# Optimization experiments

Measured on AMD Instinct MI355X. Metric: run time of the kernel, lower is better.

Reference implementation:

```python
import jax, jax.numpy as jnp
import numpy as np

D_MODEL = 768
NUM_HEADS = 12
D_K = D_MODEL // NUM_HEADS


def setup_inputs() -> dict:
    key = jax.random.key(0)
    k1, k2, k3 = jax.random.split(key, 3)
    s = 1.0 / np.sqrt(D_MODEL)
    return {
        "x": jax.random.normal(k1, (4, 2048, D_MODEL), dtype=jnp.float32),
        "W_qkv": jax.random.normal(k2, (D_MODEL, 3 * D_MODEL), dtype=jnp.float32) * s,
        "b_qkv": jnp.zeros((3 * D_MODEL,), dtype=jnp.float32),
        "W_out": jax.random.normal(k3, (D_MODEL, D_MODEL), dtype=jnp.float32) * s,
        "b_out": jnp.zeros((D_MODEL,), dtype=jnp.float32),
    }


def reference(x, W_qkv, b_qkv, W_out, b_out):
    B, S, _ = x.shape
    # fused QKV projection: [B,S,3*d_model]
    qkv = x @ W_qkv + b_qkv
    # reshape to [B,S,H,3*d_k] then to [B,H,S,3*d_k] (matches torch permute)
    qkv = qkv.reshape(B, S, NUM_HEADS, 3 * D_K).transpose(0, 2, 1, 3)
    q, k, v = jnp.split(qkv, 3, axis=-1)  # each [B,H,S,d_k]
    scale = 1.0 / jnp.sqrt(jnp.float32(D_K))
    scores = jnp.einsum("bhqd,bhkd->bhqk", q, k) * scale
    attn = jax.nn.softmax(scores, axis=-1)
    context = jnp.einsum("bhqk,bhkd->bhqd", attn, v)
    context = context.transpose(0, 2, 1, 3).reshape(B, S, D_MODEL)
    return context @ W_out + b_out
```

## Files before the change

kernel.cpp:

```cpp
#include <hip/hip_runtime.h>
#include <hip/hip_bf16.h>
#include <math.h>

#define D_MODEL 768
#define NUM_HEADS 12
#define D_K 64
#define SEQ 2048
#define BATCH 4
#define QKV_N 2304

#define QSCALE 0.18033688011112042f

typedef _Float16 f16;
typedef f16 f16x4 __attribute__((ext_vector_type(4)));
typedef f16 f16x8 __attribute__((ext_vector_type(8)));
typedef float f32x4 __attribute__((ext_vector_type(4)));

#if __has_builtin(__builtin_amdgcn_exp2f)
#define EXP2F(x) __builtin_amdgcn_exp2f(x)
#else
#define EXP2F(x) __expf(0.6931471805599453f * (x))
#endif

__device__ __forceinline__ void gload_lds16(const f16* g, f16* l) {
  __builtin_amdgcn_global_load_lds(
      (const __attribute__((address_space(1))) void*)g,
      (__attribute__((address_space(3))) void*)l, 16, 0, 0);
}

__device__ inline void xcd_swizzle(int& bx, int& by) {
  const int nx = gridDim.x;
  const int nwg = nx * gridDim.y;
  const int bidlin = blockIdx.y * nx + blockIdx.x;
  const int cpx = nwg >> 3;
  const int wg = (bidlin & 7) * cpx + (bidlin >> 3);
  bx = wg % nx;
  by = wg / nx;
}

__global__ __launch_bounds__(256) void prep_all(
    const float* __restrict__ x, const float* __restrict__ Wq,
    const float* __restrict__ Wo, f16* __restrict__ xh,
    f16* __restrict__ Wqt, f16* __restrict__ Wot) {
  const int bid = blockIdx.x;
  const int tid = threadIdx.x;
  __shared__ f16 t[64][72];

  if (bid < 1536) {
    const int idx = bid * 256 + tid;
#pragma unroll
    for (int i = 0; i < 2; ++i) {
      const size_t c = (size_t)idx + (size_t)i * 393216;
      const float4 a = *(const float4*)(x + c * 8);
      const float4 b = *(const float4*)(x + c * 8 + 4);
      f16x8 h = { (f16)a.x, (f16)a.y, (f16)a.z, (f16)a.w,
                  (f16)b.x, (f16)b.y, (f16)b.z, (f16)b.w };
      *(f16x8*)(xh + c * 8) = h;
    }
    return;
  }

  const float* W;
  f16* Wt;
  int K, N, n0, k0;
  if (bid < 1968) {
    const int tt = bid - 1536;
    W = Wq; Wt = Wqt; K = 768; N = QKV_N;
    n0 = (tt % 36) * 64; k0 = (tt / 36) * 64;
  } else {
    const int tt = bid - 1968;
    W = Wo; Wt = Wot; K = 768; N = D_MODEL;
    n0 = (tt % 12) * 64; k0 = (tt / 12) * 64;
  }

#pragma unroll
  for (int i = 0; i < 4; ++i) {
    const int slot = tid + i * 256;
    const int r = slot >> 4;
    const int c4 = (slot & 15) * 4;
    const float4 v = *(const float4*)(W + (size_t)(k0 + r) * N + n0 + c4);
    t[c4 + 0][r] = (f16)v.x;
    t[c4 + 1][r] = (f16)v.y;
    t[c4 + 2][r] = (f16)v.z;
    t[c4 + 3][r] = (f16)v.w;
  }
  __syncthreads();
#pragma unroll
  for (int i = 0; i < 2; ++i) {
    const int slot = tid + i * 256;
    const int n = slot >> 3;
    const int kc = (slot & 7) * 8;
    *(f16x8*)(Wt + (size_t)(n0 + n) * K + k0 + kc) = *(const f16x8*)(&t[n][kc]);
  }
}

#define GEMM_CORE(A_, B_, K_)                                               \
  __shared__ f16 Als[128 * 32];                                             \
  __shared__ f16 Bls[128 * 32];                                             \
  f32x4 acc[4][4];                                                          \
  _Pragma("unroll") for (int i = 0; i < 4; ++i)                             \
      _Pragma("unroll") for (int j = 0; j < 4; ++j)                         \
          acc[i][j] = (f32x4){0.f, 0.f, 0.f, 0.f};                          \
  const int sr = w * 32 + (lane >> 2);                                      \
  const int sc = (lane & 3) * 8;                                            \
  const f16* gA0 = A_ + (size_t)(bm + sr) * K_ + sc;                        \
  const f16* gA1 = gA0 + (size_t)16 * K_;                                   \
  const f16* gB0 = B_ + (size_t)(bn + sr) * K_ + sc;                        \
  const f16* gB1 = gB0 + (size_t)16 * K_;                                   \
  f16* lA0 = Als + (w * 32) * 32;                                           \
  f16* lA1 = lA0 + 16 * 32;                                                 \
  f16* lB0 = Bls + (w * 32) * 32;                                           \
  f16* lB1 = lB0 + 16 * 32;                                                 \
  for (int k0 = 0; k0 < K_; k0 += 32) {                                     \
    gload_lds16(gA0 + k0, lA0);                                             \
    gload_lds16(gA1 + k0, lA1);                                             \
    gload_lds16(gB0 + k0, lB0);                                             \
    gload_lds16(gB1 + k0, lB1);                                             \
    __syncthreads();                                                        \
    f16x8 af[4], bf[4];                                                     \
    _Pragma("unroll") for (int mi = 0; mi < 4; ++mi)                        \
        af[mi] = *(const f16x8*)(Als + (wr * 64 + mi * 16 + c) * 32 + g * 8); \
    _Pragma("unroll") for (int nj = 0; nj < 4; ++nj)                        \
        bf[nj] = *(const f16x8*)(Bls + (wc * 64 + nj * 16 + c) * 32 + g * 8); \
    _Pragma("unroll") for (int mi = 0; mi < 4; ++mi)                        \
        _Pragma("unroll") for (int nj = 0; nj < 4; ++nj)                    \
            acc[mi][nj] = __builtin_amdgcn_mfma_f32_16x16x32_f16(           \
                af[mi], bf[nj], acc[mi][nj], 0, 0, 0);                      \
    __syncthreads();                                                        \
  }

__global__ __launch_bounds__(256) void gemm_qkv(
    const f16* __restrict__ A, const f16* __restrict__ B,
    const float* __restrict__ bias,
    f16* __restrict__ Qh, f16* __restrict__ Kh, f16* __restrict__ Vt) {
  int bx, by;
  xcd_swizzle(bx, by);
  const int bm = by * 128;
  const int bn = bx * 128;
  const int tid = threadIdx.x;
  const int lane = tid & 63;
  const int w = tid >> 6;
  const int wr = w >> 1;
  const int wc = w & 1;
  const int c = lane & 15;
  const int g = lane >> 4;

  GEMM_CORE(A, B, 768)

  const int crow = g * 4;
  const int ccol = c;
#pragma unroll
  for (int nj = 0; nj < 4; ++nj) {
    const int col = bn + wc * 64 + nj * 16 + ccol;
    const int h = col / 192;
    const int rem = col - h * 192;
    const int sub = rem >> 6;
    const int d = rem & 63;
    const float bv = bias[col];
#pragma unroll
    for (int mi = 0; mi < 4; ++mi) {
      const int tok0 = bm + wr * 64 + mi * 16 + crow;
      const int b = tok0 >> 11;
      const int t0 = tok0 & 2047;
      const int bh = b * NUM_HEADS + h;
      if (sub == 2) {
        f16x4 pv = { (f16)(acc[mi][nj][0] + bv), (f16)(acc[mi][nj][1] + bv),
                     (f16)(acc[mi][nj][2] + bv), (f16)(acc[mi][nj][3] + bv) };
        *(f16x4*)(Vt + ((size_t)bh * 64 + d) * SEQ + t0) = pv;
      } else if (sub == 0) {
#pragma unroll
        for (int r = 0; r < 4; ++r)
          Qh[((size_t)bh * SEQ + t0 + r) * 64 + d] =
              (f16)((acc[mi][nj][r] + bv) * QSCALE);
      } else {
#pragma unroll
        for (int r = 0; r < 4; ++r)
          Kh[((size_t)bh * SEQ + t0 + r) * 64 + d] =
              (f16)(acc[mi][nj][r] + bv);
      }
    }
  }
}

__global__ __launch_bounds__(256) void gemm_out(
    const f16* __restrict__ A, const f16* __restrict__ B,
    const float* __restrict__ bias, float* __restrict__ C) {
  int bx, by;
  xcd_swizzle(bx, by);
  const int bm = by * 128;
  const int bn = bx * 128;
  const int tid = threadIdx.x;
  const int lane = tid & 63;
  const int w = tid >> 6;
  const int wr = w >> 1;
  const int wc = w & 1;
  const int c = lane & 15;
  const int g = lane >> 4;

  GEMM_CORE(A, B, 768)

  const int crow = g * 4;
  const int ccol = c;
#pragma unroll
  for (int nj = 0; nj < 4; ++nj) {
    const int col = bn + wc * 64 + nj * 16 + ccol;
    const float bv = bias[col];
#pragma unroll
    for (int mi = 0; mi < 4; ++mi) {
      const int rbase = bm + wr * 64 + mi * 16 + crow;
#pragma unroll
      for (int r = 0; r < 4; ++r) {
        C[(size_t)(rbase + r) * D_MODEL + col] = acc[mi][nj][r] + bv;
      }
    }
  }
}

#define COMPUTE_TILE(KL_, VL_)                                              \
  {                                                                         \
    f32x4 s_[4];                                                            \
    _Pragma("unroll") for (int mt = 0; mt < 4; ++mt)                        \
        s_[mt] = (f32x4){0.f, 0.f, 0.f, 0.f};                               \
    __builtin_amdgcn_s_setprio(1);                                          \
    _Pragma("unroll") for (int s2 = 0; s2 < 2; ++s2) {                      \
      _Pragma("unroll") for (int mt = 0; mt < 4; ++mt) {                    \
        const int row = mt * 16 + c;                                        \
        const f16x8 kf = *(const f16x8*)(KL_ + row * 64 +                   \
                         ((s2 * 32 + g * 8) ^ ((row & 7) << 3)));           \
        s_[mt] = __builtin_amdgcn_mfma_f32_16x16x32_f16(                    \
            kf, qf[s2], s_[mt], 0, 0, 0);                                   \
      }                                                                     \
    }                                                                       \
    __builtin_amdgcn_s_setprio(0);                                          \
    float tm = -INFINITY;                                                   \
    _Pragma("unroll") for (int mt = 0; mt < 4; ++mt)                        \
        _Pragma("unroll") for (int r = 0; r < 4; ++r)                       \
            tm = fmaxf(tm, s_[mt][r]);                                      \
    tm = fmaxf(tm, __shfl_xor(tm, 16));                                     \
    tm = fmaxf(tm, __shfl_xor(tm, 32));                                     \
    if (!__all(tm <= m_)) {                                                 \
      const float mn2 = fmaxf(m_, tm);                                      \
      const float sc2 = EXP2F(m_ - mn2);                                    \
      m_ = mn2;                                                             \
      l_ *= sc2;                                                            \
      _Pragma("unroll") for (int dt = 0; dt < 4; ++dt) o[dt] *= sc2;        \
    }                                                                       \
    const float mn = m_;                                                    \
    float rs = 0.f;                                                         \
    _Pragma("unroll") for (int mt = 0; mt < 4; ++mt) {                      \
      f32x4 e;                                                              \
      _Pragma("unroll") for (int r = 0; r < 4; ++r) {                       \
        e[r] = EXP2F(s_[mt][r] - mn);                                       \
        rs += e[r];                                                         \
      }                                                                     \
      s_[mt] = e;                                                           \
    }                                                                       \
    rs += __shfl_xor(rs, 16);                                               \
    rs += __shfl_xor(rs, 32);                                               \
    l_ += rs;                                                               \
    _Pragma("unroll") for (int mt = 0; mt < 4; ++mt) {                      \
      f16x4 pk = { (f16)s_[mt][0], (f16)s_[mt][1],                          \
                   (f16)s_[mt][2], (f16)s_[mt][3] };                        \
      *(f16x4*)(&Pl[w][c * 64 + ((mt * 16 + g * 4) ^ ((c & 7) << 3))]) = pk;\
    }                                                                       \
    __builtin_amdgcn_s_setprio(1);                                          \
    _Pragma("unroll") for (int s2 = 0; s2 < 2; ++s2) {                      \
      const f16x8 pf = *(const f16x8*)(&Pl[w][c * 64 +                      \
                        ((s2 * 32 + g * 8) ^ ((c & 7) << 3))]);             \
      _Pragma("unroll") for (int dt = 0; dt < 4; ++dt) {                    \
        const int row = dt * 16 + c;                                        \
        const f16x8 vf = *(const f16x8*)(VL_ + row * 64 +                   \
                         ((s2 * 32 + g * 8) ^ ((row & 7) << 3)));           \
        o[dt] = __builtin_amdgcn_mfma_f32_16x16x32_f16(                     \
            vf, pf, o[dt], 0, 0, 0);                                        \
      }                                                                     \
    }                                                                       \
    __builtin_amdgcn_s_setprio(0);                                          \
  }

__global__ __launch_bounds__(512, 6) void flash_attn_mfma(
    const f16* __restrict__ Qh, const f16* __restrict__ Kh,
    const f16* __restrict__ Vt, f16* __restrict__ ctxh) {
  const int qt = blockIdx.x, h = blockIdx.y, b = blockIdx.z;
  const int bh = b * NUM_HEADS + h;
  const int q0 = qt * 128;
  const int tid = threadIdx.x;
  const int lane = tid & 63;
  const int w = tid >> 6;
  const int c = lane & 15;
  const int g = lane >> 4;

  __shared__ f16 QPl[128 * 64];
  __shared__ f16 Kl[64 * 64];
  __shared__ f16 Vl[64 * 64];
  __shared__ f16 Pl[8][16 * 64];
  f16* Ql = QPl;
  f16* KB = QPl;
  f16* VB = QPl + 64 * 64;

  const f16* Kbase = Kh + (size_t)bh * SEQ * 64;
  const f16* Vbase = Vt + (size_t)bh * 64 * SEQ;

  const int srow = tid >> 3;
  const int sg8 = (tid & 7) * 8;
  const int sswz = sg8 ^ ((srow & 7) << 3);

#pragma unroll
  for (int ii = 0; ii < 2; ++ii) {
    const int slot = tid + ii * 512;
    const int row = slot >> 3;
    const int g8 = (slot & 7) * 8;
    f16x8 hq = *(const f16x8*)(Qh + ((size_t)bh * SEQ + q0 + row) * 64 + g8);
    *(f16x8*)(Ql + row * 64 + (g8 ^ ((row & 7) << 3))) = hq;
  }
  {
    f16x8 hk = *(const f16x8*)(Kbase + (size_t)srow * 64 + sg8);
    *(f16x8*)(Kl + srow * 64 + sswz) = hk;
    f16x8 hv = *(const f16x8*)(Vbase + (size_t)srow * SEQ + sg8);
    *(f16x8*)(Vl + srow * 64 + sswz) = hv;
  }
  __syncthreads();

  f16x8 qf[2];
#pragma unroll
  for (int s = 0; s < 2; ++s) {
    const int row = w * 16 + c;
    qf[s] = *(const f16x8*)(Ql + row * 64 +
                            ((s * 32 + g * 8) ^ ((row & 7) << 3)));
  }
  __syncthreads();

  {
    f16x8 hk = *(const f16x8*)(Kbase + (size_t)64 * 64 + (size_t)srow * 64 + sg8);
    *(f16x8*)(KB + srow * 64 + sswz) = hk;
    f16x8 hv = *(const f16x8*)(Vbase + (size_t)srow * SEQ + 64 + sg8);
    *(f16x8*)(VB + srow * 64 + sswz) = hv;
  }
  __syncthreads();

  f32x4 o[4];
  float m_ = -INFINITY, l_ = 0.f;
#pragma unroll
  for (int dt = 0; dt < 4; ++dt) o[dt] = (f32x4){0.f, 0.f, 0.f, 0.f};

  for (int pt = 0; pt < SEQ / 128; ++pt) {
    f16x8 nkA, nvA, nkB, nvB;
    const bool more = (pt + 1) < SEQ / 128;
    if (more) {
      const int tA = 2 * pt + 2, tB = 2 * pt + 3;
      nkA = *(const f16x8*)(Kbase + (size_t)tA * 64 * 64 + (size_t)srow * 64 + sg8);
      nvA = *(const f16x8*)(Vbase + (size_t)srow * SEQ + tA * 64 + sg8);
      nkB = *(const f16x8*)(Kbase + (size_t)tB * 64 * 64 + (size_t)srow * 64 + sg8);
      nvB = *(const f16x8*)(Vbase + (size_t)srow * SEQ + tB * 64 + sg8);
    }

    COMPUTE_TILE(Kl, Vl)
    COMPUTE_TILE(KB, VB)

    __syncthreads();

    if (more) {
      *(f16x8*)(Kl + srow * 64 + sswz) = nkA;
      *(f16x8*)(Vl + srow * 64 + sswz) = nvA;
      *(f16x8*)(KB + srow * 64 + sswz) = nkB;
      *(f16x8*)(VB + srow * 64 + sswz) = nvB;
    }
    __syncthreads();
  }

  {
    const float inv = 1.f / l_;
    const int q = q0 + w * 16 + c;
#pragma unroll
    for (int dt = 0; dt < 4; ++dt) {
      f16x4 r4 = { (f16)(o[dt][0] * inv), (f16)(o[dt][1] * inv),
                   (f16)(o[dt][2] * inv), (f16)(o[dt][3] * inv) };
      *(f16x4*)(ctxh + ((size_t)(b * SEQ) + q) * D_MODEL + h * 64 +
                dt * 16 + g * 4) = r4;
    }
  }
}

extern "C" void kernel_launch(void* const* d_in, const int* in_sizes, int n_in,
                              void* d_out, int out_size, void* d_ws, size_t ws_size,
                              hipStream_t stream) {
  const float* x     = (const float*)d_in[0];
  const float* W_qkv = (const float*)d_in[1];
  const float* b_qkv = (const float*)d_in[2];
  const float* W_out = (const float*)d_in[3];
  const float* b_out = (const float*)d_in[4];
  float* out = (float*)d_out;

  const int M = BATCH * SEQ;
  const int BH = BATCH * NUM_HEADS;

  f16* xh   = (f16*)d_ws;
  f16* Wqt  = xh + (size_t)M * D_MODEL;
  f16* Wot  = Wqt + (size_t)QKV_N * D_MODEL;
  f16* Qh   = Wot + (size_t)D_MODEL * D_MODEL;
  f16* Kh   = Qh + (size_t)BH * SEQ * 64;
  f16* Vt   = Kh + (size_t)BH * SEQ * 64;
  f16* ctxh = Vt + (size_t)BH * SEQ * 64;

  dim3 block(256);

  hipLaunchKernelGGL(prep_all, dim3(2112), block, 0, stream,
                     x, W_qkv, W_out, xh, Wqt, Wot);

  hipLaunchKernelGGL(gemm_qkv, dim3(QKV_N / 128, M / 128), block, 0, stream,
                     xh, Wqt, b_qkv, Qh, Kh, Vt);

  hipLaunchKernelGGL(flash_attn_mfma, dim3(SEQ / 128, NUM_HEADS, BATCH),
                     dim3(512), 0, stream, Qh, Kh, Vt, ctxh);

  hipLaunchKernelGGL(gemm_out, dim3(D_MODEL / 128, M / 128), block, 0, stream,
                     ctxh, Wot, b_out, out);
}
```

Baseline: 178.1 us.

## Pipeline K/V loads per tile and remap attention grid for L2 locality

The attention loop now handles one 64-key tile per step instead of two. Each step prefetches only the next tile into registers and writes it into the buffer it has just finished with, with one barrier per step. This holds fewer prefetch registers at a time and drops the extra barrier per 128 keys, at the cost of more frequent synchronisation. The 3D grid also becomes a 1D grid whose index interleaves batch-head across the low bits, so blocks that share the same K/V likely land together (presumably the same XCD), aiming for better L2 reuse.

```diff
diff --git a/kernel.cpp b/kernel.cpp
--- a/kernel.cpp
+++ b/kernel.cpp
@@ -216,8 +216,16 @@
   }
 }
 
-#define COMPUTE_TILE(KL_, VL_)                                              \
+#define ATTN_STEP(KL_, VL_, TLOAD_)                                         \
   {                                                                         \
+    f16x8 nk, nv;                                                           \
+    const bool more = (TLOAD_) < SEQ / 64;                                  \
+    if (more) {                                                             \
+      nk = *(const f16x8*)(Kbase + (size_t)(TLOAD_) * 64 * 64 +             \
+                           (size_t)srow * 64 + sg8);                        \
+      nv = *(const f16x8*)(Vbase + (size_t)srow * SEQ + (TLOAD_) * 64 +     \
+                           sg8);                                            \
+    }                                                                       \
     f32x4 s_[4];                                                            \
     _Pragma("unroll") for (int mt = 0; mt < 4; ++mt)                        \
         s_[mt] = (f32x4){0.f, 0.f, 0.f, 0.f};                               \
@@ -276,13 +284,22 @@
       }                                                                     \
     }                                                                       \
     __builtin_amdgcn_s_setprio(0);                                          \
+    __syncthreads();                                                        \
+    if (more) {                                                             \
+      *(f16x8*)(KL_ + srow * 64 + sswz) = nk;                               \
+      *(f16x8*)(VL_ + srow * 64 + sswz) = nv;                               \
+    }                                                                       \
   }
 
 __global__ __launch_bounds__(512, 6) void flash_attn_mfma(
     const f16* __restrict__ Qh, const f16* __restrict__ Kh,
     const f16* __restrict__ Vt, f16* __restrict__ ctxh) {
-  const int qt = blockIdx.x, h = blockIdx.y, b = blockIdx.z;
-  const int bh = b * NUM_HEADS + h;
+  const int i = blockIdx.x;
+  const int j = i >> 3;
+  const int bh = (i & 7) + 8 * (j >> 4);
+  const int qt = j & 15;
+  const int b = bh / NUM_HEADS;
+  const int h = bh - b * NUM_HEADS;
   const int q0 = qt * 128;
   const int tid = threadIdx.x;
   const int lane = tid & 63;
@@ -291,12 +308,13 @@
   const int g = lane >> 4;
 
   __shared__ f16 QPl[128 * 64];
-  __shared__ f16 Kl[64 * 64];
-  __shared__ f16 Vl[64 * 64];
+  __shared__ f16 KV0[2 * 64 * 64];
   __shared__ f16 Pl[8][16 * 64];
   f16* Ql = QPl;
-  f16* KB = QPl;
-  f16* VB = QPl + 64 * 64;
+  f16* K0 = KV0;
+  f16* V0 = KV0 + 64 * 64;
+  f16* K1 = QPl;
+  f16* V1 = QPl + 64 * 64;
 
   const f16* Kbase = Kh + (size_t)bh * SEQ * 64;
   const f16* Vbase = Vt + (size_t)bh * 64 * SEQ;
@@ -315,9 +333,9 @@
   }
   {
     f16x8 hk = *(const f16x8*)(Kbase + (size_t)srow * 64 + sg8);
-    *(f16x8*)(Kl + srow * 64 + sswz) = hk;
+    *(f16x8*)(K0 + srow * 64 + sswz) = hk;
     f16x8 hv = *(const f16x8*)(Vbase + (size_t)srow * SEQ + sg8);
-    *(f16x8*)(Vl + srow * 64 + sswz) = hv;
+    *(f16x8*)(V0 + srow * 64 + sswz) = hv;
   }
   __syncthreads();
 
@@ -332,40 +350,19 @@
 
   {
     f16x8 hk = *(const f16x8*)(Kbase + (size_t)64 * 64 + (size_t)srow * 64 + sg8);
-    *(f16x8*)(KB + srow * 64 + sswz) = hk;
+    *(f16x8*)(K1 + srow * 64 + sswz) = hk;
     f16x8 hv = *(const f16x8*)(Vbase + (size_t)srow * SEQ + 64 + sg8);
-    *(f16x8*)(VB + srow * 64 + sswz) = hv;
-  }
-  __syncthreads();
+    *(f16x8*)(V1 + srow * 64 + sswz) = hv;
+  }
 
   f32x4 o[4];
   float m_ = -INFINITY, l_ = 0.f;
 #pragma unroll
   for (int dt = 0; dt < 4; ++dt) o[dt] = (f32x4){0.f, 0.f, 0.f, 0.f};
 
-  for (int pt = 0; pt < SEQ / 128; ++pt) {
-    f16x8 nkA, nvA, nkB, nvB;
-    const bool more = (pt + 1) < SEQ / 128;
-    if (more) {
-      const int tA = 2 * pt + 2, tB = 2 * pt + 3;
-      nkA = *(const f16x8*)(Kbase + (size_t)tA * 64 * 64 + (size_t)srow * 64 + sg8);
-      nvA = *(const f16x8*)(Vbase + (size_t)srow * SEQ + tA * 64 + sg8);
-      nkB = *(const f16x8*)(Kbase + (size_t)tB * 64 * 64 + (size_t)srow * 64 + sg8);
-      nvB = *(const f16x8*)(Vbase + (size_t)srow * SEQ + tB * 64 + sg8);
-    }
-
-    COMPUTE_TILE(Kl, Vl)
-    COMPUTE_TILE(KB, VB)
-
-    __syncthreads();
-
-    if (more) {
-      *(f16x8*)(Kl + srow * 64 + sswz) = nkA;
-      *(f16x8*)(Vl + srow * 64 + sswz) = nvA;
-      *(f16x8*)(KB + srow * 64 + sswz) = nkB;
-      *(f16x8*)(VB + srow * 64 + sswz) = nvB;
-    }
-    __syncthreads();
+  for (int kt = 0; kt < SEQ / 64; kt += 2) {
+    ATTN_STEP(K0, V0, kt + 2)
+    ATTN_STEP(K1, V1, kt + 3)
   }
 
   {
@@ -410,7 +407,7 @@
   hipLaunchKernelGGL(gemm_qkv, dim3(QKV_N / 128, M / 128), block, 0, stream,
                      xh, Wqt, b_qkv, Qh, Kh, Vt);
 
-  hipLaunchKernelGGL(flash_attn_mfma, dim3(SEQ / 128, NUM_HEADS, BATCH),
+  hipLaunchKernelGGL(flash_attn_mfma, dim3(16 * NUM_HEADS * BATCH),
                      dim3(512), 0, stream, Qh, Kh, Vt, ctxh);
 
   hipLaunchKernelGGL(gemm_out, dim3(D_MODEL / 128, M / 128), block, 0, stream,
```

Result: slower. 186.8 us (+4.9%).
